# Kernel tuning notes

Hardware: AMD Instinct MI355X
Metric: run time of the kernel (lower is better)

## Reference

```python
import jax, jax.numpy as jnp
import numpy as np

DIM = 512      # dim_token
H = 8          # nheads
EH = DIM // H  # head dim
MAXT = 512     # max_time_id
NBUCK = 2 * MAXT - 1  # relative-position buckets


def rope(x, t):
    # x: [N,H,L,E], t: [N,L] integer time ids
    half = x.shape[-1] // 2
    inv_freq = 1.0 / (10000.0 ** (jnp.arange(half, dtype=jnp.float32) / half))
    ang = t.astype(jnp.float32)[:, None, :, None] * inv_freq  # [N,1,L,half]
    cos, sin = jnp.cos(ang), jnp.sin(ang)
    x1, x2 = x[..., :half], x[..., half:]
    return jnp.concatenate([x1 * cos - x2 * sin, x2 * cos + x1 * sin], axis=-1)


def setup_inputs() -> dict:
    key = jax.random.key(0)
    ks = jax.random.split(key, 8)
    N, L = 4, 1024
    x = jax.random.normal(ks[0], (N, L, DIM), dtype=jnp.float32)
    mask = jnp.ones((N, L), dtype=bool)
    time_ids = jnp.sort(jax.random.randint(ks[1], (N, L), 0, MAXT), axis=-1)
    s = DIM ** -0.5
    W_in = jax.random.normal(ks[2], (3 * DIM, DIM), dtype=jnp.float32) * s
    b_in = jnp.zeros((3 * DIM,), dtype=jnp.float32)
    W_out = jax.random.normal(ks[3], (DIM, DIM), dtype=jnp.float32) * s
    b_out = jnp.zeros((DIM,), dtype=jnp.float32)
    rel_table = jax.random.normal(ks[4], (H, NBUCK), dtype=jnp.float32) * 0.02
    post_table = jax.random.normal(ks[5], (H, NBUCK), dtype=jnp.float32) * 0.02
    return dict(x=x, mask=mask, time_ids=time_ids, W_in=W_in, b_in=b_in,
                W_out=W_out, b_out=b_out, rel_table=rel_table, post_table=post_table)


def reference(x, mask, time_ids, W_in, b_in, W_out, b_out, rel_table, post_table):
    N, L, _ = x.shape
    # 1. input projection, chunk into q,k,v
    qkv = x @ W_in.T + b_in
    q, k, v = jnp.split(qkv, 3, axis=-1)
    split = lambda t: t.reshape(N, L, H, EH).transpose(0, 2, 1, 3)  # [N,H,L,EH]
    q, k, v = split(q), split(k), split(v)
    # 2. RoPE on q,k using time_ids (pe_module.apply_attention_pe)
    q = rope(q, time_ids)
    k = rope(k, time_ids)
    # relative time-difference bucket indices [N,L,L]
    diff = time_ids[:, :, None] - time_ids[:, None, :]
    idx = jnp.clip(diff + (MAXT - 1), 0, NBUCK - 1)
    bias = rel_table[:, idx].transpose(1, 0, 2, 3)        # [N,H,L,L] pre-softmax bias
    post_bias = post_table[:, idx].transpose(1, 0, 2, 3)  # [N,H,L,L] EfficientRPE post-softmax
    # 3. manual attention path (bias is not None -> bypass SDPA)
    scale = EH ** -0.5
    scores = jnp.einsum('bhqe,bhke->bhqk', q, k) * scale + bias
    am = mask[:, None, None, :]  # [N,1,1,L]
    scores = jnp.where(am, scores, -jnp.inf)
    w = jax.nn.softmax(scores, axis=-1)
    out = jnp.einsum('bhqk,bhke->bhqe', w, v)
    # EfficientRPE post-softmax correction
    post_bias = jnp.where(am, post_bias, 0.0)
    out = out + jnp.einsum('bhql,bhle->bhqe', post_bias, v)
    # 4. merge heads + output projection
    out = out.transpose(0, 2, 1, 3).reshape(N, L, DIM)
    return out @ W_out.T + b_out
```

## Files before the change

### kernel.cpp

```cpp
#include <hip/hip_runtime.h>
#include <hip/hip_bf16.h>

#define BB 4
#define LL 1024
#define DIMD 512
#define HH 8
#define EHD 64
#define NBUCK 1023

using f32x4 = __attribute__((ext_vector_type(4))) float;
using s16x8 = __attribute__((ext_vector_type(8))) short;

__device__ __forceinline__ ushort to_bf16(float x) {
    union { float f; unsigned u; } v; v.f = x;
    unsigned r = (v.u + 0x7FFFu + ((v.u >> 16) & 1u)) >> 16;
    return (ushort)r;
}

__device__ __forceinline__ unsigned cvt_pk_bf16(float lo, float hi) {
    unsigned r;
    asm("v_cvt_pk_bf16_f32 %0, %1, %2" : "=v"(r) : "v"(lo), "v"(hi));
    return r;
}

__device__ __forceinline__ void gl_lds16(const ushort* g, ushort* l) {
    __builtin_amdgcn_global_load_lds(
        (const __attribute__((address_space(1))) unsigned int*)g,
        (__attribute__((address_space(3))) unsigned int*)l, 16, 0, 0);
}

#define XN  2097152
#define WIN 786432
#define WON 262144
__global__ __launch_bounds__(256) void prep_all(const float* __restrict__ x,
                                                const float* __restrict__ wi,
                                                const float* __restrict__ wo,
                                                ushort* __restrict__ xb,
                                                ushort* __restrict__ wib,
                                                ushort* __restrict__ wob,
                                                float2* __restrict__ rtab)
{
    if (blockIdx.x < 3072) {
        int idx = (blockIdx.x * 256 + threadIdx.x) * 4;
        const float* src; ushort* dst; int off;
        if (idx < XN)            { src = x;  dst = xb;  off = idx; }
        else if (idx < XN + WIN) { src = wi; dst = wib; off = idx - XN; }
        else                     { src = wo; dst = wob; off = idx - XN - WIN; }
        float4 v = *(const float4*)&src[off];
        ushort4 o;
        o.x = to_bf16(v.x); o.y = to_bf16(v.y);
        o.z = to_bf16(v.z); o.w = to_bf16(v.w);
        *(ushort4*)&dst[off] = o;
    } else {
        int idx = (blockIdx.x - 3072) * 256 + threadIdx.x;
        int tt = idx >> 5, e = idx & 31;
        const float L2T = 13.287712379549449f;
        float inv = exp2f(-(float)e * (L2T / 32.f));
        float ang = (float)tt * inv;
        float s, c;
        sincosf(ang, &s, &c);
        rtab[idx] = make_float2(c, s);
    }
}

template<int BN, int WMODE>
__global__ __launch_bounds__(256) void mfma_gemm(const ushort* __restrict__ A,
                                                 const ushort* __restrict__ B,
                                                 const float* __restrict__ bias,
                                                 float* __restrict__ outf,
                                                 ushort* __restrict__ outq,
                                                 ushort* __restrict__ outk,
                                                 ushort* __restrict__ outv,
                                                 const int* __restrict__ time_ids,
                                                 const float2* __restrict__ rtab,
                                                 int M, int N, int K)
{
    constexpr int NREP = BN / 32;
    constexpr int BUFU = 8192 + BN * 64;
    __shared__ __align__(16) char smem[2 * BUFU * 2];
    ushort* base = (ushort*)smem;

    const int t = threadIdx.x;
    const int lane = t & 63;
    const int w = t >> 6;
    const int l15 = lane & 15, lg = lane >> 4;
    const int wr = w >> 1, wc = w & 1;
    const int m0 = blockIdx.x * 128;
    const int n0 = blockIdx.y * BN;

    const int asub = lane >> 3;
    const int kc8 = (lane & 7) * 8;
    const int arow_base = w * 32;
    const int brow_base = w * (BN / 4);

    f32x4 acc[4][NREP];
    #pragma unroll
    for (int mf = 0; mf < 4; ++mf)
        #pragma unroll
        for (int nf = 0; nf < NREP; ++nf)
            acc[mf][nf] = {0.f, 0.f, 0.f, 0.f};

    #define STAGE_G(BUF, K0)                                                          \
        do {                                                                          \
            ushort* Ab = base + (BUF) * BUFU;                                         \
            ushort* Bb = Ab + 8192;                                                   \
            _Pragma("unroll")                                                         \
            for (int i = 0; i < 4; ++i) {                                             \
                int row = arow_base + i * 8;                                          \
                gl_lds16(&A[(size_t)(m0 + row + asub) * K + (K0) + kc8], &Ab[row * 64]); \
            }                                                                         \
            _Pragma("unroll")                                                         \
            for (int i = 0; i < BN / 32; ++i) {                                       \
                int row = brow_base + i * 8;                                          \
                gl_lds16(&B[(size_t)(n0 + row + asub) * K + (K0) + kc8], &Bb[row * 64]); \
            }                                                                         \
        } while (0)

    STAGE_G(0, 0);
    __syncthreads();

    for (int k0 = 0; k0 < K; k0 += 64) {
        const int buf = (k0 >> 6) & 1;
        if (k0 + 64 < K) {
            STAGE_G(buf ^ 1, k0 + 64);
            if constexpr (BN == 128) asm volatile("s_waitcnt vmcnt(8)" ::: "memory");
            else                     asm volatile("s_waitcnt vmcnt(6)" ::: "memory");
        } else {
            asm volatile("s_waitcnt vmcnt(0)" ::: "memory");
        }
        __builtin_amdgcn_s_barrier();
        ushort* Abuf = base + buf * BUFU;
        ushort* Bbuf = Abuf + 8192;
        #pragma unroll
        for (int kk = 0; kk < 2; ++kk) {
            s16x8 af[4], bf[NREP];
            #pragma unroll
            for (int mf = 0; mf < 4; ++mf)
                af[mf] = *(const s16x8*)&Abuf[(wr * 64 + mf * 16 + l15) * 64 + kk * 32 + lg * 8];
            #pragma unroll
            for (int nf = 0; nf < NREP; ++nf)
                bf[nf] = *(const s16x8*)&Bbuf[(wc * (BN / 2) + nf * 16 + l15) * 64 + kk * 32 + lg * 8];
            __builtin_amdgcn_s_setprio(1);
            #pragma unroll
            for (int mf = 0; mf < 4; ++mf)
                #pragma unroll
                for (int nf = 0; nf < NREP; ++nf)
                    acc[mf][nf] = __builtin_amdgcn_mfma_f32_16x16x32_bf16(af[mf], bf[nf], acc[mf][nf], 0, 0, 0);
            __builtin_amdgcn_s_setprio(0);
        }
        asm volatile("" ::: "memory");
        __builtin_amdgcn_s_barrier();
    }

    if (WMODE == 0) {
        float bv[NREP];
        #pragma unroll
        for (int nf = 0; nf < NREP; ++nf) bv[nf] = bias[n0 + wc * (BN / 2) + nf * 16 + l15];
        #pragma unroll
        for (int mf = 0; mf < 4; ++mf)
            #pragma unroll
            for (int r = 0; r < 4; ++r) {
                int m = m0 + wr * 64 + mf * 16 + lg * 4 + r;
                #pragma unroll
                for (int nf = 0; nf < NREP; ++nf)
                    outf[(size_t)m * N + n0 + wc * (BN / 2) + nf * 16 + l15] = acc[mf][nf][r] + bv[nf];
            }
    } else {
        const int which = n0 >> 9;
        if (which < 2) {
            const int h = ((n0 & 511) + wc * 64) >> 6;
            ushort* dst = (which == 0) ? outq : outk;
            float bv[4];
            #pragma unroll
            for (int nf = 0; nf < 4; ++nf) bv[nf] = bias[n0 + wc * 64 + nf * 16 + l15];
            #pragma unroll
            for (int mf = 0; mf < 4; ++mf)
                #pragma unroll
                for (int r = 0; r < 4; ++r) {
                    int m = m0 + wr * 64 + mf * 16 + lg * 4 + r;
                    int b = m >> 10, li = m & (LL - 1);
                    int tt = time_ids[b * LL + li];
                    size_t rowbase = (((size_t)(b * HH + h)) * LL + li) * EHD;
                    #pragma unroll
                    for (int nf = 0; nf < 2; ++nf) {
                        float2 cs = rtab[tt * 32 + nf * 16 + l15];
                        float v1 = acc[mf][nf][r] + bv[nf];
                        float v2 = acc[mf][nf + 2][r] + bv[nf + 2];
                        dst[rowbase + nf * 16 + l15]      = to_bf16(v1 * cs.x - v2 * cs.y);
                        dst[rowbase + 32 + nf * 16 + l15] = to_bf16(v2 * cs.x + v1 * cs.y);
                    }
                }
        } else {
            ushort* T = (ushort*)smem;
            float bv[4];
            #pragma unroll
            for (int nf = 0; nf < 4; ++nf) bv[nf] = bias[n0 + wc * 64 + nf * 16 + l15];
            #pragma unroll
            for (int mf = 0; mf < 4; ++mf)
                #pragma unroll
                for (int nf = 0; nf < 4; ++nf) {
                    int n = wc * 64 + nf * 16 + l15;
                    int mb = wr * 64 + mf * 16 + lg * 4;
                    ushort4 pk;
                    pk.x = to_bf16(acc[mf][nf][0] + bv[nf]);
                    pk.y = to_bf16(acc[mf][nf][1] + bv[nf]);
                    pk.z = to_bf16(acc[mf][nf][2] + bv[nf]);
                    pk.w = to_bf16(acc[mf][nf][3] + bv[nf]);
                    *(ushort4*)&T[n * 136 + mb] = pk;
                }
            __syncthreads();
            const int b = m0 >> 10, li0 = m0 & (LL - 1);
            const int hbase = (n0 & 511) >> 6;
            #pragma unroll
            for (int it = 0; it < 8; ++it) {
                int n = it * 16 + (t >> 4);
                int mc = (t & 15) * 8;
                uint4 val = *(const uint4*)&T[n * 136 + mc];
                int h = hbase + (n >> 6);
                int e = n & 63;
                *(uint4*)&outv[(((size_t)(b * HH + h)) * EHD + e) * LL + li0 + mc] = val;
            }
        }
    }
}

__global__ __launch_bounds__(512, 4) void attn_mfma(const ushort* __restrict__ qb,
                                                    const ushort* __restrict__ kb,
                                                    const ushort* __restrict__ vt,
                                                    const int* __restrict__ time_ids,
                                                    const float* __restrict__ rel_table,
                                                    const float* __restrict__ post_table,
                                                    ushort* __restrict__ ao)
{
    __shared__ __align__(16) char smem[65536];
    __shared__ __align__(16) float rt_s[1024];
    __shared__ __align__(16) float pt_s[1024];
    __shared__ __align__(16) int   tid4_s[1024];

    const int t = threadIdx.x;
    const int lane = t & 63;
    const int w = t >> 6;
    const int wh = w & 3;
    const int half = w >> 2;
    const int l15 = lane & 15, lg = lane >> 4;

    const int wg = blockIdx.x;
    const int xcd = wg & 7;
    const int j = wg >> 3;
    const int bh = xcd * 4 + (j & 3);
    const int qt = j >> 2;
    const int b = bh >> 3, h = bh & 7;
    const int wq0 = qt * 64 + wh * 16;

    ushort* Kh = (ushort*)smem + half * 8192;
    ushort* Vh = (ushort*)(smem + 32768) + half * 8192;

    const float L2E = 1.4426950408889634f;
    const float M0 = 12.0f;
    for (int i = t; i < NBUCK; i += 512) {
        rt_s[i] = rel_table[h * NBUCK + i] * L2E - M0;
        pt_s[i] = post_table[h * NBUCK + i];
    }
    const int* tid_b = time_ids + b * LL;
    #pragma unroll
    for (int i = 0; i < 2; ++i) tid4_s[i * 512 + t] = tid_b[i * 512 + t] * 4;

    const ushort* qpan = qb + (size_t)bh * LL * EHD;
    const ushort* kpan = kb + (size_t)bh * LL * EHD;
    const ushort* vpan = vt + (size_t)bh * EHD * LL;

    s16x8 qf[2];
    #pragma unroll
    for (int ec = 0; ec < 2; ++ec)
        qf[ec] = *(const s16x8*)&qpan[(size_t)(wq0 + l15) * EHD + ec * 32 + lg * 8];

    const int tqA4 = (tid_b[wq0 + l15] + 511) * 4;

    const int srow = lane >> 3;
    const int sswz = (lane & 7) ^ srow;

    #define STAGE(BUF, K0)                                                        \
        do {                                                                      \
            int r0 = wh * 8 + srow;                                               \
            gl_lds16(&kpan[(size_t)((K0) + r0) * EHD + sswz * 8],      &Kh[(BUF) * 4096 + wh * 8 * 64]);        \
            gl_lds16(&vpan[(size_t)r0 * LL + (K0) + sswz * 8],         &Vh[(BUF) * 4096 + wh * 8 * 64]);        \
            gl_lds16(&kpan[(size_t)((K0) + r0 + 32) * EHD + sswz * 8], &Kh[(BUF) * 4096 + (32 + wh * 8) * 64]); \
            gl_lds16(&vpan[(size_t)(r0 + 32) * LL + (K0) + sswz * 8],  &Vh[(BUF) * 4096 + (32 + wh * 8) * 64]); \
        } while (0)

    float dreg = 0.f;
    f32x4 ot[4], o2[4];
    #pragma unroll
    for (int ei = 0; ei < 4; ++ei) {
        ot[ei] = {0.f, 0.f, 0.f, 0.f};
        o2[ei] = {0.f, 0.f, 0.f, 0.f};
    }

    const int ktbase = half * 8;
    STAGE(0, ktbase * 64);
    __syncthreads();

    const int srcA = ((lg & 1) << 5) + l15;
    const bool hi = (lg & 2) != 0;

    for (int i = 0; i < 8; ++i) {
        const int cur = i & 1;
        const int k0 = (ktbase + i) * 64;
        if (i < 7) {
            STAGE(cur ^ 1, k0 + 64);
            asm volatile("s_waitcnt vmcnt(4)" ::: "memory");
        } else {
            asm volatile("s_waitcnt vmcnt(0)" ::: "memory");
        }
        __builtin_amdgcn_s_barrier();

        const char* Kc = (const char*)&Kh[cur * 4096];
        const char* Vc = (const char*)&Vh[cur * 4096];

        f32x4 sc[4];
        #pragma unroll
        for (int ci = 0; ci < 4; ++ci) sc[ci] = {0.f, 0.f, 0.f, 0.f};
        __builtin_amdgcn_s_setprio(1);
        #pragma unroll
        for (int ec = 0; ec < 2; ++ec)
            #pragma unroll
            for (int ci = 0; ci < 4; ++ci) {
                int row = ci * 16 + l15;
                s16x8 kf = *(const s16x8*)(Kc + row * 128 +
                                           ((ec * 64 + lg * 16) ^ ((row & 7) << 4)));
                sc[ci] = __builtin_amdgcn_mfma_f32_16x16x32_bf16(kf, qf[ec], sc[ci], 0, 0, 0);
            }
        __builtin_amdgcn_s_setprio(0);

        s16x8 vf[4][2];
        #pragma unroll
        for (int ei = 0; ei < 4; ++ei)
            #pragma unroll
            for (int kk = 0; kk < 2; ++kk) {
                int row = ei * 16 + l15;
                vf[ei][kk] = *(const s16x8*)(Vc + row * 128 +
                                             ((kk * 64 + lg * 16) ^ ((row & 7) << 4)));
            }

        #pragma unroll
        for (int kk = 0; kk < 2; ++kk) {
            int4 ta = *(const int4*)&tid4_s[k0 + kk * 32 + lg * 8];
            int4 tb = *(const int4*)&tid4_s[k0 + kk * 32 + lg * 8 + 4];
            float p0 = *(const float*)((const char*)pt_s + (tqA4 - ta.x));
            float p1 = *(const float*)((const char*)pt_s + (tqA4 - ta.y));
            float p2 = *(const float*)((const char*)pt_s + (tqA4 - ta.z));
            float p3 = *(const float*)((const char*)pt_s + (tqA4 - ta.w));
            float p4 = *(const float*)((const char*)pt_s + (tqA4 - tb.x));
            float p5 = *(const float*)((const char*)pt_s + (tqA4 - tb.y));
            float p6 = *(const float*)((const char*)pt_s + (tqA4 - tb.z));
            float p7 = *(const float*)((const char*)pt_s + (tqA4 - tb.w));
            union { unsigned u[4]; s16x8 v; } pbu;
            pbu.u[0] = cvt_pk_bf16(p0, p1);
            pbu.u[1] = cvt_pk_bf16(p2, p3);
            pbu.u[2] = cvt_pk_bf16(p4, p5);
            pbu.u[3] = cvt_pk_bf16(p6, p7);
            __builtin_amdgcn_s_setprio(1);
            #pragma unroll
            for (int ei = 0; ei < 4; ++ei)
                o2[ei] = __builtin_amdgcn_mfma_f32_16x16x32_bf16(vf[ei][kk], pbu.v, o2[ei], 0, 0, 0);
            __builtin_amdgcn_s_setprio(0);
        }

        float rsum = 0.f;
        #pragma unroll
        for (int ci = 0; ci < 4; ++ci) {
            int4 tk4 = *(const int4*)&tid4_s[k0 + ci * 16 + lg * 4];
            float p0 = exp2f(sc[ci][0] * 0.18033688011111793f + *(const float*)((const char*)rt_s + (tqA4 - tk4.x)));
            float p1 = exp2f(sc[ci][1] * 0.18033688011111793f + *(const float*)((const char*)rt_s + (tqA4 - tk4.y)));
            float p2 = exp2f(sc[ci][2] * 0.18033688011111793f + *(const float*)((const char*)rt_s + (tqA4 - tk4.z)));
            float p3 = exp2f(sc[ci][3] * 0.18033688011111793f + *(const float*)((const char*)rt_s + (tqA4 - tk4.w)));
            sc[ci][0] = p0; sc[ci][1] = p1; sc[ci][2] = p2; sc[ci][3] = p3;
            rsum += (p0 + p1) + (p2 + p3);
        }
        dreg += rsum;

        unsigned pk[4][2];
        #pragma unroll
        for (int ci = 0; ci < 4; ++ci) {
            pk[ci][0] = cvt_pk_bf16(sc[ci][0], sc[ci][1]);
            pk[ci][1] = cvt_pk_bf16(sc[ci][2], sc[ci][3]);
        }

        #pragma unroll
        for (int kk = 0; kk < 2; ++kk) {
            unsigned a0 = __shfl(pk[kk * 2][0], srcA),      b0 = __shfl(pk[kk * 2 + 1][0], srcA);
            unsigned a1 = __shfl(pk[kk * 2][1], srcA),      b1 = __shfl(pk[kk * 2 + 1][1], srcA);
            unsigned a2 = __shfl(pk[kk * 2][0], srcA + 16), b2 = __shfl(pk[kk * 2 + 1][0], srcA + 16);
            unsigned a3 = __shfl(pk[kk * 2][1], srcA + 16), b3 = __shfl(pk[kk * 2 + 1][1], srcA + 16);
            union { unsigned u[4]; s16x8 v; } pb;
            pb.u[0] = hi ? b0 : a0;
            pb.u[1] = hi ? b1 : a1;
            pb.u[2] = hi ? b2 : a2;
            pb.u[3] = hi ? b3 : a3;
            __builtin_amdgcn_s_setprio(1);
            #pragma unroll
            for (int ei = 0; ei < 4; ++ei)
                ot[ei] = __builtin_amdgcn_mfma_f32_16x16x32_bf16(vf[ei][kk], pb.v, ot[ei], 0, 0, 0);
            __builtin_amdgcn_s_setprio(0);
        }

        asm volatile("" ::: "memory");
        __builtin_amdgcn_s_barrier();
    }

    dreg += __shfl_xor(dreg, 16);
    dreg += __shfl_xor(dreg, 32);

    float* mergeO = (float*)smem;
    float* mergeB = (float*)(smem + 17408);
    float* mergeD = (float*)(smem + 34816);
    const int mrow = wh * 16 + l15;

    if (half == 1) {
        #pragma unroll
        for (int ei = 0; ei < 4; ++ei) {
            *(float4*)&mergeO[mrow * 68 + ei * 16 + lg * 4] =
                make_float4(ot[ei][0], ot[ei][1], ot[ei][2], ot[ei][3]);
            *(float4*)&mergeB[mrow * 68 + ei * 16 + lg * 4] =
                make_float4(o2[ei][0], o2[ei][1], o2[ei][2], o2[ei][3]);
        }
        if (lg == 0) mergeD[mrow] = dreg;
    }
    __syncthreads();

    if (half == 0) {
        float invd = 1.f / (dreg + mergeD[mrow]);
        const size_t orow = (size_t)(b * LL + wq0 + l15) * DIMD + h * EHD;
        #pragma unroll
        for (int ei = 0; ei < 4; ++ei) {
            float4 o1 = *(const float4*)&mergeO[mrow * 68 + ei * 16 + lg * 4];
            float4 b1 = *(const float4*)&mergeB[mrow * 68 + ei * 16 + lg * 4];
            ushort4 st;
            st.x = to_bf16((ot[ei][0] + o1.x) * invd + o2[ei][0] + b1.x);
            st.y = to_bf16((ot[ei][1] + o1.y) * invd + o2[ei][1] + b1.y);
            st.z = to_bf16((ot[ei][2] + o1.z) * invd + o2[ei][2] + b1.z);
            st.w = to_bf16((ot[ei][3] + o1.w) * invd + o2[ei][3] + b1.w);
            *(ushort4*)&ao[orow + ei * 16 + lg * 4] = st;
        }
    }
}

extern "C" void kernel_launch(void* const* d_in, const int* in_sizes, int n_in,
                              void* d_out, int out_size, void* d_ws, size_t ws_size,
                              hipStream_t stream)
{
    const float* x        = (const float*)d_in[0];
    const int*   time_ids = (const int*)d_in[2];
    const float* W_in     = (const float*)d_in[3];
    const float* b_in     = (const float*)d_in[4];
    const float* W_out    = (const float*)d_in[5];
    const float* b_out    = (const float*)d_in[6];
    const float* rel_t    = (const float*)d_in[7];
    const float* post_t   = (const float*)d_in[8];
    float* out = (float*)d_out;

    ushort* wsu = (ushort*)d_ws;
    ushort* xb  = wsu;
    ushort* wib = xb + XN;
    ushort* wob = wib + WIN;
    ushort* qbf = wob + WON;
    ushort* kbf = qbf + XN;
    ushort* vtb = kbf + XN;
    ushort* aob = vtb + XN;
    float2* rtab = (float2*)(aob + XN);

    prep_all<<<3136, 256, 0, stream>>>(x, W_in, W_out, xb, wib, wob, rtab);
    mfma_gemm<128, 1><<<dim3(32, 12), 256, 0, stream>>>(xb, wib, b_in,
                                                        nullptr, qbf, kbf, vtb,
                                                        time_ids, (const float2*)rtab,
                                                        BB * LL, 3 * DIMD, DIMD);
    attn_mfma<<<512, 512, 0, stream>>>(qbf, kbf, vtb, time_ids,
                                       rel_t, post_t, aob);
    mfma_gemm<64, 0><<<dim3(32, 8), 256, 0, stream>>>(aob, wob, b_out,
                                                      out, nullptr, nullptr, nullptr,
                                                      nullptr, nullptr,
                                                      BB * LL, DIMD, DIMD);
}
```

Baseline: 64.64 us.

## Process two 16-row query groups per wave to reuse K/V LDS fragments

Each wave now handles 32 query rows (two groups of 16) instead of 16, so every K and V fragment read from LDS feeds twice as many MFMAs. The grid is halved to 256 blocks and the launch bound drops to 2 blocks per CU to make room for the doubled accumulators and K fragments held in registers. The intent is to cut LDS traffic and K/V staging per unit of work, at the cost of higher register pressure, fewer blocks than CUs, and a serialized two-pass merge epilogue.

```diff
diff --git a/kernel.cpp b/kernel.cpp
--- a/kernel.cpp
+++ b/kernel.cpp
@@ -224,7 +224,7 @@
     }
 }
 
-__global__ __launch_bounds__(512, 4) void attn_mfma(const ushort* __restrict__ qb,
+__global__ __launch_bounds__(512, 2) void attn_mfma(const ushort* __restrict__ qb,
                                                     const ushort* __restrict__ kb,
                                                     const ushort* __restrict__ vt,
                                                     const int* __restrict__ time_ids,
@@ -250,7 +250,7 @@
     const int bh = xcd * 4 + (j & 3);
     const int qt = j >> 2;
     const int b = bh >> 3, h = bh & 7;
-    const int wq0 = qt * 64 + wh * 16;
+    const int wq0 = qt * 128 + wh * 32;
 
     ushort* Kh = (ushort*)smem + half * 8192;
     ushort* Vh = (ushort*)(smem + 32768) + half * 8192;
@@ -269,12 +269,15 @@
     const ushort* kpan = kb + (size_t)bh * LL * EHD;
     const ushort* vpan = vt + (size_t)bh * EHD * LL;
 
-    s16x8 qf[2];
+    s16x8 qf[2][2];
     #pragma unroll
-    for (int ec = 0; ec < 2; ++ec)
-        qf[ec] = *(const s16x8*)&qpan[(size_t)(wq0 + l15) * EHD + ec * 32 + lg * 8];
-
-    const int tqA4 = (tid_b[wq0 + l15] + 511) * 4;
+    for (int g = 0; g < 2; ++g)
+        #pragma unroll
+        for (int ec = 0; ec < 2; ++ec)
+            qf[g][ec] = *(const s16x8*)&qpan[(size_t)(wq0 + g * 16 + l15) * EHD + ec * 32 + lg * 8];
+
+    const int tqA4[2] = {(tid_b[wq0 + l15] + 511) * 4,
+                         (tid_b[wq0 + 16 + l15] + 511) * 4};
 
     const int srow = lane >> 3;
     const int sswz = (lane & 7) ^ srow;
@@ -288,13 +291,15 @@
             gl_lds16(&vpan[(size_t)(r0 + 32) * LL + (K0) + sswz * 8],  &Vh[(BUF) * 4096 + (32 + wh * 8) * 64]); \
         } while (0)
 
-    float dreg = 0.f;
-    f32x4 ot[4], o2[4];
+    float dreg[2] = {0.f, 0.f};
+    f32x4 ot[2][4], o2[2][4];
     #pragma unroll
-    for (int ei = 0; ei < 4; ++ei) {
-        ot[ei] = {0.f, 0.f, 0.f, 0.f};
-        o2[ei] = {0.f, 0.f, 0.f, 0.f};
-    }
+    for (int g = 0; g < 2; ++g)
+        #pragma unroll
+        for (int ei = 0; ei < 4; ++ei) {
+            ot[g][ei] = {0.f, 0.f, 0.f, 0.f};
+            o2[g][ei] = {0.f, 0.f, 0.f, 0.f};
+        }
 
     const int ktbase = half * 8;
     STAGE(0, ktbase * 64);
@@ -317,19 +322,29 @@
         const char* Kc = (const char*)&Kh[cur * 4096];
         const char* Vc = (const char*)&Vh[cur * 4096];
 
-        f32x4 sc[4];
-        #pragma unroll
-        for (int ci = 0; ci < 4; ++ci) sc[ci] = {0.f, 0.f, 0.f, 0.f};
+        s16x8 kf[4][2];
+        #pragma unroll
+        for (int ci = 0; ci < 4; ++ci)
+            #pragma unroll
+            for (int ec = 0; ec < 2; ++ec) {
+                int row = ci * 16 + l15;
+                kf[ci][ec] = *(const s16x8*)(Kc + row * 128 +
+                                             ((ec * 64 + lg * 16) ^ ((row & 7) << 4)));
+            }
+
+        f32x4 sc[2][4];
+        #pragma unroll
+        for (int g = 0; g < 2; ++g)
+            #pragma unroll
+            for (int ci = 0; ci < 4; ++ci) sc[g][ci] = {0.f, 0.f, 0.f, 0.f};
         __builtin_amdgcn_s_setprio(1);
         #pragma unroll
         for (int ec = 0; ec < 2; ++ec)
             #pragma unroll
-            for (int ci = 0; ci < 4; ++ci) {
-                int row = ci * 16 + l15;
-                s16x8 kf = *(const s16x8*)(Kc + row * 128 +
-                                           ((ec * 64 + lg * 16) ^ ((row & 7) << 4)));
-                sc[ci] = __builtin_amdgcn_mfma_f32_16x16x32_bf16(kf, qf[ec], sc[ci], 0, 0, 0);
-            }
+            for (int ci = 0; ci < 4; ++ci)
+                #pragma unroll
+                for (int g = 0; g < 2; ++g)
+                    sc[g][ci] = __builtin_amdgcn_mfma_f32_16x16x32_bf16(kf[ci][ec], qf[g][ec], sc[g][ci], 0, 0, 0);
         __builtin_amdgcn_s_setprio(0);
 
         s16x8 vf[4][2];
@@ -346,101 +361,118 @@
         for (int kk = 0; kk < 2; ++kk) {
             int4 ta = *(const int4*)&tid4_s[k0 + kk * 32 + lg * 8];
             int4 tb = *(const int4*)&tid4_s[k0 + kk * 32 + lg * 8 + 4];
-            float p0 = *(const float*)((const char*)pt_s + (tqA4 - ta.x));
-            float p1 = *(const float*)((const char*)pt_s + (tqA4 - ta.y));
-            float p2 = *(const float*)((const char*)pt_s + (tqA4 - ta.z));
-            float p3 = *(const float*)((const char*)pt_s + (tqA4 - ta.w));
-            float p4 = *(const float*)((const char*)pt_s + (tqA4 - tb.x));
-            float p5 = *(const float*)((const char*)pt_s + (tqA4 - tb.y));
-            float p6 = *(const float*)((const char*)pt_s + (tqA4 - tb.z));
-            float p7 = *(const float*)((const char*)pt_s + (tqA4 - tb.w));
-            union { unsigned u[4]; s16x8 v; } pbu;
-            pbu.u[0] = cvt_pk_bf16(p0, p1);
-            pbu.u[1] = cvt_pk_bf16(p2, p3);
-            pbu.u[2] = cvt_pk_bf16(p4, p5);
-            pbu.u[3] = cvt_pk_bf16(p6, p7);
-            __builtin_amdgcn_s_setprio(1);
-            #pragma unroll
-            for (int ei = 0; ei < 4; ++ei)
-                o2[ei] = __builtin_amdgcn_mfma_f32_16x16x32_bf16(vf[ei][kk], pbu.v, o2[ei], 0, 0, 0);
-            __builtin_amdgcn_s_setprio(0);
-        }
-
-        float rsum = 0.f;
+            #pragma unroll
+            for (int g = 0; g < 2; ++g) {
+                float p0 = *(const float*)((const char*)pt_s + (tqA4[g] - ta.x));
+                float p1 = *(const float*)((const char*)pt_s + (tqA4[g] - ta.y));
+                float p2 = *(const float*)((const char*)pt_s + (tqA4[g] - ta.z));
+                float p3 = *(const float*)((const char*)pt_s + (tqA4[g] - ta.w));
+                float p4 = *(const float*)((const char*)pt_s + (tqA4[g] - tb.x));
+                float p5 = *(const float*)((const char*)pt_s + (tqA4[g] - tb.y));
+                float p6 = *(const float*)((const char*)pt_s + (tqA4[g] - tb.z));
+                float p7 = *(const float*)((const char*)pt_s + (tqA4[g] - tb.w));
+                union { unsigned u[4]; s16x8 v; } pbu;
+                pbu.u[0] = cvt_pk_bf16(p0, p1);
+                pbu.u[1] = cvt_pk_bf16(p2, p3);
+                pbu.u[2] = cvt_pk_bf16(p4, p5);
+                pbu.u[3] = cvt_pk_bf16(p6, p7);
+                __builtin_amdgcn_s_setprio(1);
+                #pragma unroll
+                for (int ei = 0; ei < 4; ++ei)
+                    o2[g][ei] = __builtin_amdgcn_mfma_f32_16x16x32_bf16(vf[ei][kk], pbu.v, o2[g][ei], 0, 0, 0);
+                __builtin_amdgcn_s_setprio(0);
+            }
+        }
+
+        float rsum[2] = {0.f, 0.f};
         #pragma unroll
         for (int ci = 0; ci < 4; ++ci) {
             int4 tk4 = *(const int4*)&tid4_s[k0 + ci * 16 + lg * 4];
-            float p0 = exp2f(sc[ci][0] * 0.18033688011111793f + *(const float*)((const char*)rt_s + (tqA4 - tk4.x)));
-            float p1 = exp2f(sc[ci][1] * 0.18033688011111793f + *(const float*)((const char*)rt_s + (tqA4 - tk4.y)));
-            float p2 = exp2f(sc[ci][2] * 0.18033688011111793f + *(const float*)((const char*)rt_s + (tqA4 - tk4.z)));
-            float p3 = exp2f(sc[ci][3] * 0.18033688011111793f + *(const float*)((const char*)rt_s + (tqA4 - tk4.w)));
-            sc[ci][0] = p0; sc[ci][1] = p1; sc[ci][2] = p2; sc[ci][3] = p3;
-            rsum += (p0 + p1) + (p2 + p3);
-        }
-        dreg += rsum;
-
-        unsigned pk[4][2];
-        #pragma unroll
-        for (int ci = 0; ci < 4; ++ci) {
-            pk[ci][0] = cvt_pk_bf16(sc[ci][0], sc[ci][1]);
-            pk[ci][1] = cvt_pk_bf16(sc[ci][2], sc[ci][3]);
-        }
-
-        #pragma unroll
-        for (int kk = 0; kk < 2; ++kk) {
-            unsigned a0 = __shfl(pk[kk * 2][0], srcA),      b0 = __shfl(pk[kk * 2 + 1][0], srcA);
-            unsigned a1 = __shfl(pk[kk * 2][1], srcA),      b1 = __shfl(pk[kk * 2 + 1][1], srcA);
-            unsigned a2 = __shfl(pk[kk * 2][0], srcA + 16), b2 = __shfl(pk[kk * 2 + 1][0], srcA + 16);
-            unsigned a3 = __shfl(pk[kk * 2][1], srcA + 16), b3 = __shfl(pk[kk * 2 + 1][1], srcA + 16);
-            union { unsigned u[4]; s16x8 v; } pb;
-            pb.u[0] = hi ? b0 : a0;
-            pb.u[1] = hi ? b1 : a1;
-            pb.u[2] = hi ? b2 : a2;
-            pb.u[3] = hi ? b3 : a3;
-            __builtin_amdgcn_s_setprio(1);
-            #pragma unroll
-            for (int ei = 0; ei < 4; ++ei)
-                ot[ei] = __builtin_amdgcn_mfma_f32_16x16x32_bf16(vf[ei][kk], pb.v, ot[ei], 0, 0, 0);
-            __builtin_amdgcn_s_setprio(0);
-        }
+            #pragma unroll
+            for (int g = 0; g < 2; ++g) {
+                float p0 = exp2f(sc[g][ci][0] * 0.18033688011111793f + *(const float*)((const char*)rt_s + (tqA4[g] - tk4.x)));
+                float p1 = exp2f(sc[g][ci][1] * 0.18033688011111793f + *(const float*)((const char*)rt_s + (tqA4[g] - tk4.y)));
+                float p2 = exp2f(sc[g][ci][2] * 0.18033688011111793f + *(const float*)((const char*)rt_s + (tqA4[g] - tk4.z)));
+                float p3 = exp2f(sc[g][ci][3] * 0.18033688011111793f + *(const float*)((const char*)rt_s + (tqA4[g] - tk4.w)));
+                sc[g][ci][0] = p0; sc[g][ci][1] = p1; sc[g][ci][2] = p2; sc[g][ci][3] = p3;
+                rsum[g] += (p0 + p1) + (p2 + p3);
+            }
+        }
+        dreg[0] += rsum[0];
+        dreg[1] += rsum[1];
+
+        unsigned pk[2][4][2];
+        #pragma unroll
+        for (int g = 0; g < 2; ++g)
+            #pragma unroll
+            for (int ci = 0; ci < 4; ++ci) {
+                pk[g][ci][0] = cvt_pk_bf16(sc[g][ci][0], sc[g][ci][1]);
+                pk[g][ci][1] = cvt_pk_bf16(sc[g][ci][2], sc[g][ci][3]);
+            }
+
+        #pragma unroll
+        for (int g = 0; g < 2; ++g)
+            #pragma unroll
+            for (int kk = 0; kk < 2; ++kk) {
+                unsigned a0 = __shfl(pk[g][kk * 2][0], srcA),      b0 = __shfl(pk[g][kk * 2 + 1][0], srcA);
+                unsigned a1 = __shfl(pk[g][kk * 2][1], srcA),      b1 = __shfl(pk[g][kk * 2 + 1][1], srcA);
+                unsigned a2 = __shfl(pk[g][kk * 2][0], srcA + 16), b2 = __shfl(pk[g][kk * 2 + 1][0], srcA + 16);
+                unsigned a3 = __shfl(pk[g][kk * 2][1], srcA + 16), b3 = __shfl(pk[g][kk * 2 + 1][1], srcA + 16);
+                union { unsigned u[4]; s16x8 v; } pb;
+                pb.u[0] = hi ? b0 : a0;
+                pb.u[1] = hi ? b1 : a1;
+                pb.u[2] = hi ? b2 : a2;
+                pb.u[3] = hi ? b3 : a3;
+                __builtin_amdgcn_s_setprio(1);
+                #pragma unroll
+                for (int ei = 0; ei < 4; ++ei)
+                    ot[g][ei] = __builtin_amdgcn_mfma_f32_16x16x32_bf16(vf[ei][kk], pb.v, ot[g][ei], 0, 0, 0);
+                __builtin_amdgcn_s_setprio(0);
+            }
 
         asm volatile("" ::: "memory");
         __builtin_amdgcn_s_barrier();
     }
 
-    dreg += __shfl_xor(dreg, 16);
-    dreg += __shfl_xor(dreg, 32);
+    #pragma unroll
+    for (int g = 0; g < 2; ++g) {
+        dreg[g] += __shfl_xor(dreg[g], 16);
+        dreg[g] += __shfl_xor(dreg[g], 32);
+    }
 
     float* mergeO = (float*)smem;
     float* mergeB = (float*)(smem + 17408);
     float* mergeD = (float*)(smem + 34816);
     const int mrow = wh * 16 + l15;
 
-    if (half == 1) {
-        #pragma unroll
-        for (int ei = 0; ei < 4; ++ei) {
-            *(float4*)&mergeO[mrow * 68 + ei * 16 + lg * 4] =
-                make_float4(ot[ei][0], ot[ei][1], ot[ei][2], ot[ei][3]);
-            *(float4*)&mergeB[mrow * 68 + ei * 16 + lg * 4] =
-                make_float4(o2[ei][0], o2[ei][1], o2[ei][2], o2[ei][3]);
-        }
-        if (lg == 0) mergeD[mrow] = dreg;
-    }
-    __syncthreads();
-
-    if (half == 0) {
-        float invd = 1.f / (dreg + mergeD[mrow]);
-        const size_t orow = (size_t)(b * LL + wq0 + l15) * DIMD + h * EHD;
-        #pragma unroll
-        for (int ei = 0; ei < 4; ++ei) {
-            float4 o1 = *(const float4*)&mergeO[mrow * 68 + ei * 16 + lg * 4];
-            float4 b1 = *(const float4*)&mergeB[mrow * 68 + ei * 16 + lg * 4];
-            ushort4 st;
-            st.x = to_bf16((ot[ei][0] + o1.x) * invd + o2[ei][0] + b1.x);
-            st.y = to_bf16((ot[ei][1] + o1.y) * invd + o2[ei][1] + b1.y);
-            st.z = to_bf16((ot[ei][2] + o1.z) * invd + o2[ei][2] + b1.z);
-            st.w = to_bf16((ot[ei][3] + o1.w) * invd + o2[ei][3] + b1.w);
-            *(ushort4*)&ao[orow + ei * 16 + lg * 4] = st;
+    #pragma unroll
+    for (int g = 0; g < 2; ++g) {
+        __syncthreads();
+        if (half == 1) {
+            #pragma unroll
+            for (int ei = 0; ei < 4; ++ei) {
+                *(float4*)&mergeO[mrow * 68 + ei * 16 + lg * 4] =
+                    make_float4(ot[g][ei][0], ot[g][ei][1], ot[g][ei][2], ot[g][ei][3]);
+                *(float4*)&mergeB[mrow * 68 + ei * 16 + lg * 4] =
+                    make_float4(o2[g][ei][0], o2[g][ei][1], o2[g][ei][2], o2[g][ei][3]);
+            }
+            if (lg == 0) mergeD[mrow] = dreg[g];
+        }
+        __syncthreads();
+        if (half == 0) {
+            float invd = 1.f / (dreg[g] + mergeD[mrow]);
+            const size_t orow = (size_t)(b * LL + wq0 + g * 16 + l15) * DIMD + h * EHD;
+            #pragma unroll
+            for (int ei = 0; ei < 4; ++ei) {
+                float4 o1 = *(const float4*)&mergeO[mrow * 68 + ei * 16 + lg * 4];
+                float4 b1 = *(const float4*)&mergeB[mrow * 68 + ei * 16 + lg * 4];
+                ushort4 st;
+                st.x = to_bf16((ot[g][ei][0] + o1.x) * invd + o2[g][ei][0] + b1.x);
+                st.y = to_bf16((ot[g][ei][1] + o1.y) * invd + o2[g][ei][1] + b1.y);
+                st.z = to_bf16((ot[g][ei][2] + o1.z) * invd + o2[g][ei][2] + b1.z);
+                st.w = to_bf16((ot[g][ei][3] + o1.w) * invd + o2[g][ei][3] + b1.w);
+                *(ushort4*)&ao[orow + ei * 16 + lg * 4] = st;
+            }
         }
     }
 }
@@ -474,7 +506,7 @@
                                                         nullptr, qbf, kbf, vtb,
                                                         time_ids, (const float2*)rtab,
                                                         BB * LL, 3 * DIMD, DIMD);
-    attn_mfma<<<512, 512, 0, stream>>>(qbf, kbf, vtb, time_ids,
+    attn_mfma<<<256, 512, 0, stream>>>(qbf, kbf, vtb, time_ids,
                                        rel_t, post_t, aob);
     mfma_gemm<64, 0><<<dim3(32, 8), 256, 0, stream>>>(aob, wob, b_out,
                                                       out, nullptr, nullptr, nullptr,
```

Measured after the change: 64.11 us, median of 2. About the same (-0.8%).

## Drop split-K across wave halves in attention; 4 waves each cover full key range

Applied to the files above, without the earlier changes.

The attention kernel previously used 8 waves per block, with two halves each processing half of the keys and merging partial outputs through shared memory. Now each block has 4 waves that walk all 1024 keys, staging 128-key double-buffered tiles and processing two 64-key sub-tiles per barrier. This removes the cross-half LDS merge and halves the number of barriers per key. In exchange each wave does twice the serial work and the block has fewer waves to hide latency.

```diff
diff --git a/kernel.cpp b/kernel.cpp
--- a/kernel.cpp
+++ b/kernel.cpp
@@ -224,7 +224,7 @@
     }
 }
 
-__global__ __launch_bounds__(512, 4) void attn_mfma(const ushort* __restrict__ qb,
+__global__ __launch_bounds__(256, 2) void attn_mfma(const ushort* __restrict__ qb,
                                                     const ushort* __restrict__ kb,
                                                     const ushort* __restrict__ vt,
                                                     const int* __restrict__ time_ids,
@@ -232,7 +232,8 @@
                                                     const float* __restrict__ post_table,
                                                     ushort* __restrict__ ao)
 {
-    __shared__ __align__(16) char smem[65536];
+    __shared__ __align__(16) ushort Kbuf[2][8192];
+    __shared__ __align__(16) ushort Vbuf[2][8192];
     __shared__ __align__(16) float rt_s[1024];
     __shared__ __align__(16) float pt_s[1024];
     __shared__ __align__(16) int   tid4_s[1024];
@@ -240,8 +241,6 @@
     const int t = threadIdx.x;
     const int lane = t & 63;
     const int w = t >> 6;
-    const int wh = w & 3;
-    const int half = w >> 2;
     const int l15 = lane & 15, lg = lane >> 4;
 
     const int wg = blockIdx.x;
@@ -250,20 +249,17 @@
     const int bh = xcd * 4 + (j & 3);
     const int qt = j >> 2;
     const int b = bh >> 3, h = bh & 7;
-    const int wq0 = qt * 64 + wh * 16;
-
-    ushort* Kh = (ushort*)smem + half * 8192;
-    ushort* Vh = (ushort*)(smem + 32768) + half * 8192;
+    const int wq0 = qt * 64 + w * 16;
 
     const float L2E = 1.4426950408889634f;
     const float M0 = 12.0f;
-    for (int i = t; i < NBUCK; i += 512) {
+    for (int i = t; i < NBUCK; i += 256) {
         rt_s[i] = rel_table[h * NBUCK + i] * L2E - M0;
         pt_s[i] = post_table[h * NBUCK + i];
     }
     const int* tid_b = time_ids + b * LL;
     #pragma unroll
-    for (int i = 0; i < 2; ++i) tid4_s[i * 512 + t] = tid_b[i * 512 + t] * 4;
+    for (int i = 0; i < 4; ++i) tid4_s[i * 256 + t] = tid_b[i * 256 + t] * 4;
 
     const ushort* qpan = qb + (size_t)bh * LL * EHD;
     const ushort* kpan = kb + (size_t)bh * LL * EHD;
@@ -279,13 +275,22 @@
     const int srow = lane >> 3;
     const int sswz = (lane & 7) ^ srow;
 
-    #define STAGE(BUF, K0)                                                        \
-        do {                                                                      \
-            int r0 = wh * 8 + srow;                                               \
-            gl_lds16(&kpan[(size_t)((K0) + r0) * EHD + sswz * 8],      &Kh[(BUF) * 4096 + wh * 8 * 64]);        \
-            gl_lds16(&vpan[(size_t)r0 * LL + (K0) + sswz * 8],         &Vh[(BUF) * 4096 + wh * 8 * 64]);        \
-            gl_lds16(&kpan[(size_t)((K0) + r0 + 32) * EHD + sswz * 8], &Kh[(BUF) * 4096 + (32 + wh * 8) * 64]); \
-            gl_lds16(&vpan[(size_t)(r0 + 32) * LL + (K0) + sswz * 8],  &Vh[(BUF) * 4096 + (32 + wh * 8) * 64]); \
+    #define STAGE(BUF, K0)                                                              \
+        do {                                                                            \
+            _Pragma("unroll")                                                           \
+            for (int rr = 0; rr < 4; ++rr) {                                            \
+                int r0 = w * 8 + srow + rr * 32;                                        \
+                gl_lds16(&kpan[(size_t)((K0) + r0) * EHD + sswz * 8],                   \
+                         &Kbuf[BUF][(w * 8 + rr * 32) * 64]);                           \
+            }                                                                           \
+            _Pragma("unroll")                                                           \
+            for (int ks = 0; ks < 2; ++ks)                                              \
+                _Pragma("unroll")                                                       \
+                for (int eg = 0; eg < 2; ++eg) {                                        \
+                    int e0 = w * 8 + srow + eg * 32;                                    \
+                    gl_lds16(&vpan[(size_t)e0 * LL + (K0) + ks * 64 + sswz * 8],        \
+                             &Vbuf[BUF][ks * 4096 + (w * 8 + eg * 32) * 64]);           \
+                }                                                                       \
         } while (0)
 
     float dreg = 0.f;
@@ -296,112 +301,115 @@
         o2[ei] = {0.f, 0.f, 0.f, 0.f};
     }
 
-    const int ktbase = half * 8;
-    STAGE(0, ktbase * 64);
+    STAGE(0, 0);
     __syncthreads();
 
     const int srcA = ((lg & 1) << 5) + l15;
     const bool hi = (lg & 2) != 0;
 
-    for (int i = 0; i < 8; ++i) {
-        const int cur = i & 1;
-        const int k0 = (ktbase + i) * 64;
-        if (i < 7) {
-            STAGE(cur ^ 1, k0 + 64);
-            asm volatile("s_waitcnt vmcnt(4)" ::: "memory");
+    for (int it = 0; it < 8; ++it) {
+        const int buf = it & 1;
+        const int kbase = it * 128;
+        if (it < 7) {
+            STAGE(buf ^ 1, kbase + 128);
+            asm volatile("s_waitcnt vmcnt(8)" ::: "memory");
         } else {
             asm volatile("s_waitcnt vmcnt(0)" ::: "memory");
         }
         __builtin_amdgcn_s_barrier();
 
-        const char* Kc = (const char*)&Kh[cur * 4096];
-        const char* Vc = (const char*)&Vh[cur * 4096];
-
-        f32x4 sc[4];
         #pragma unroll
-        for (int ci = 0; ci < 4; ++ci) sc[ci] = {0.f, 0.f, 0.f, 0.f};
-        __builtin_amdgcn_s_setprio(1);
-        #pragma unroll
-        for (int ec = 0; ec < 2; ++ec)
+        for (int ks = 0; ks < 2; ++ks) {
+            const int k0 = kbase + ks * 64;
+            const char* Kc = (const char*)&Kbuf[buf][ks * 4096];
+            const char* Vc = (const char*)&Vbuf[buf][ks * 4096];
+
+            f32x4 sc[4];
+            #pragma unroll
+            for (int ci = 0; ci < 4; ++ci) sc[ci] = {0.f, 0.f, 0.f, 0.f};
+            __builtin_amdgcn_s_setprio(1);
+            #pragma unroll
+            for (int ec = 0; ec < 2; ++ec)
+                #pragma unroll
+                for (int ci = 0; ci < 4; ++ci) {
+                    int row = ci * 16 + l15;
+                    s16x8 kf = *(const s16x8*)(Kc + row * 128 +
+                                               ((ec * 64 + lg * 16) ^ ((row & 7) << 4)));
+                    sc[ci] = __builtin_amdgcn_mfma_f32_16x16x32_bf16(kf, qf[ec], sc[ci], 0, 0, 0);
+                }
+            __builtin_amdgcn_s_setprio(0);
+
+            s16x8 vf[4][2];
+            #pragma unroll
+            for (int ei = 0; ei < 4; ++ei)
+                #pragma unroll
+                for (int kk = 0; kk < 2; ++kk) {
+                    int row = ei * 16 + l15;
+                    vf[ei][kk] = *(const s16x8*)(Vc + row * 128 +
+                                                 ((kk * 64 + lg * 16) ^ ((row & 7) << 4)));
+                }
+
+            #pragma unroll
+            for (int kk = 0; kk < 2; ++kk) {
+                int4 ta = *(const int4*)&tid4_s[k0 + kk * 32 + lg * 8];
+                int4 tb = *(const int4*)&tid4_s[k0 + kk * 32 + lg * 8 + 4];
+                float p0 = *(const float*)((const char*)pt_s + (tqA4 - ta.x));
+                float p1 = *(const float*)((const char*)pt_s + (tqA4 - ta.y));
+                float p2 = *(const float*)((const char*)pt_s + (tqA4 - ta.z));
+                float p3 = *(const float*)((const char*)pt_s + (tqA4 - ta.w));
+                float p4 = *(const float*)((const char*)pt_s + (tqA4 - tb.x));
+                float p5 = *(const float*)((const char*)pt_s + (tqA4 - tb.y));
+                float p6 = *(const float*)((const char*)pt_s + (tqA4 - tb.z));
+                float p7 = *(const float*)((const char*)pt_s + (tqA4 - tb.w));
+                union { unsigned u[4]; s16x8 v; } pbu;
+                pbu.u[0] = cvt_pk_bf16(p0, p1);
+                pbu.u[1] = cvt_pk_bf16(p2, p3);
+                pbu.u[2] = cvt_pk_bf16(p4, p5);
+                pbu.u[3] = cvt_pk_bf16(p6, p7);
+                __builtin_amdgcn_s_setprio(1);
+                #pragma unroll
+                for (int ei = 0; ei < 4; ++ei)
+                    o2[ei] = __builtin_amdgcn_mfma_f32_16x16x32_bf16(vf[ei][kk], pbu.v, o2[ei], 0, 0, 0);
+                __builtin_amdgcn_s_setprio(0);
+            }
+
+            float rsum = 0.f;
             #pragma unroll
             for (int ci = 0; ci < 4; ++ci) {
-                int row = ci * 16 + l15;
-                s16x8 kf = *(const s16x8*)(Kc + row * 128 +
-                                           ((ec * 64 + lg * 16) ^ ((row & 7) << 4)));
-                sc[ci] = __builtin_amdgcn_mfma_f32_16x16x32_bf16(kf, qf[ec], sc[ci], 0, 0, 0);
-            }
-        __builtin_amdgcn_s_setprio(0);
-
-        s16x8 vf[4][2];
-        #pragma unroll
-        for (int ei = 0; ei < 4; ++ei)
+                int4 tk4 = *(const int4*)&tid4_s[k0 + ci * 16 + lg * 4];
+                float p0 = exp2f(sc[ci][0] * 0.18033688011111793f + *(const float*)((const char*)rt_s + (tqA4 - tk4.x)));
+                float p1 = exp2f(sc[ci][1] * 0.18033688011111793f + *(const float*)((const char*)rt_s + (tqA4 - tk4.y)));
+                float p2 = exp2f(sc[ci][2] * 0.18033688011111793f + *(const float*)((const char*)rt_s + (tqA4 - tk4.z)));
+                float p3 = exp2f(sc[ci][3] * 0.18033688011111793f + *(const float*)((const char*)rt_s + (tqA4 - tk4.w)));
+                sc[ci][0] = p0; sc[ci][1] = p1; sc[ci][2] = p2; sc[ci][3] = p3;
+                rsum += (p0 + p1) + (p2 + p3);
+            }
+            dreg += rsum;
+
+            unsigned pk[4][2];
+            #pragma unroll
+            for (int ci = 0; ci < 4; ++ci) {
+                pk[ci][0] = cvt_pk_bf16(sc[ci][0], sc[ci][1]);
+                pk[ci][1] = cvt_pk_bf16(sc[ci][2], sc[ci][3]);
+            }
+
             #pragma unroll
             for (int kk = 0; kk < 2; ++kk) {
-                int row = ei * 16 + l15;
-                vf[ei][kk] = *(const s16x8*)(Vc + row * 128 +
-                                             ((kk * 64 + lg * 16) ^ ((row & 7) << 4)));
-            }
-
-        #pragma unroll
-        for (int kk = 0; kk < 2; ++kk) {
-            int4 ta = *(const int4*)&tid4_s[k0 + kk * 32 + lg * 8];
-            int4 tb = *(const int4*)&tid4_s[k0 + kk * 32 + lg * 8 + 4];
-            float p0 = *(const float*)((const char*)pt_s + (tqA4 - ta.x));
-            float p1 = *(const float*)((const char*)pt_s + (tqA4 - ta.y));
-            float p2 = *(const float*)((const char*)pt_s + (tqA4 - ta.z));
-            float p3 = *(const float*)((const char*)pt_s + (tqA4 - ta.w));
-            float p4 = *(const float*)((const char*)pt_s + (tqA4 - tb.x));
-            float p5 = *(const float*)((const char*)pt_s + (tqA4 - tb.y));
-            float p6 = *(const float*)((const char*)pt_s + (tqA4 - tb.z));
-            float p7 = *(const float*)((const char*)pt_s + (tqA4 - tb.w));
-            union { unsigned u[4]; s16x8 v; } pbu;
-            pbu.u[0] = cvt_pk_bf16(p0, p1);
-            pbu.u[1] = cvt_pk_bf16(p2, p3);
-            pbu.u[2] = cvt_pk_bf16(p4, p5);
-            pbu.u[3] = cvt_pk_bf16(p6, p7);
-            __builtin_amdgcn_s_setprio(1);
-            #pragma unroll
-            for (int ei = 0; ei < 4; ++ei)
-                o2[ei] = __builtin_amdgcn_mfma_f32_16x16x32_bf16(vf[ei][kk], pbu.v, o2[ei], 0, 0, 0);
-            __builtin_amdgcn_s_setprio(0);
-        }
-
-        float rsum = 0.f;
-        #pragma unroll
-        for (int ci = 0; ci < 4; ++ci) {
-            int4 tk4 = *(const int4*)&tid4_s[k0 + ci * 16 + lg * 4];
-            float p0 = exp2f(sc[ci][0] * 0.18033688011111793f + *(const float*)((const char*)rt_s + (tqA4 - tk4.x)));
-            float p1 = exp2f(sc[ci][1] * 0.18033688011111793f + *(const float*)((const char*)rt_s + (tqA4 - tk4.y)));
-            float p2 = exp2f(sc[ci][2] * 0.18033688011111793f + *(const float*)((const char*)rt_s + (tqA4 - tk4.z)));
-            float p3 = exp2f(sc[ci][3] * 0.18033688011111793f + *(const float*)((const char*)rt_s + (tqA4 - tk4.w)));
-            sc[ci][0] = p0; sc[ci][1] = p1; sc[ci][2] = p2; sc[ci][3] = p3;
-            rsum += (p0 + p1) + (p2 + p3);
-        }
-        dreg += rsum;
-
-        unsigned pk[4][2];
-        #pragma unroll
-        for (int ci = 0; ci < 4; ++ci) {
-            pk[ci][0] = cvt_pk_bf16(sc[ci][0], sc[ci][1]);
-            pk[ci][1] = cvt_pk_bf16(sc[ci][2], sc[ci][3]);
-        }
-
-        #pragma unroll
-        for (int kk = 0; kk < 2; ++kk) {
-            unsigned a0 = __shfl(pk[kk * 2][0], srcA),      b0 = __shfl(pk[kk * 2 + 1][0], srcA);
-            unsigned a1 = __shfl(pk[kk * 2][1], srcA),      b1 = __shfl(pk[kk * 2 + 1][1], srcA);
-            unsigned a2 = __shfl(pk[kk * 2][0], srcA + 16), b2 = __shfl(pk[kk * 2 + 1][0], srcA + 16);
-            unsigned a3 = __shfl(pk[kk * 2][1], srcA + 16), b3 = __shfl(pk[kk * 2 + 1][1], srcA + 16);
-            union { unsigned u[4]; s16x8 v; } pb;
-            pb.u[0] = hi ? b0 : a0;
-            pb.u[1] = hi ? b1 : a1;
-            pb.u[2] = hi ? b2 : a2;
-            pb.u[3] = hi ? b3 : a3;
-            __builtin_amdgcn_s_setprio(1);
-            #pragma unroll
-            for (int ei = 0; ei < 4; ++ei)
-                ot[ei] = __builtin_amdgcn_mfma_f32_16x16x32_bf16(vf[ei][kk], pb.v, ot[ei], 0, 0, 0);
-            __builtin_amdgcn_s_setprio(0);
+                unsigned a0 = __shfl(pk[kk * 2][0], srcA),      b0 = __shfl(pk[kk * 2 + 1][0], srcA);
+                unsigned a1 = __shfl(pk[kk * 2][1], srcA),      b1 = __shfl(pk[kk * 2 + 1][1], srcA);
+                unsigned a2 = __shfl(pk[kk * 2][0], srcA + 16), b2 = __shfl(pk[kk * 2 + 1][0], srcA + 16);
+                unsigned a3 = __shfl(pk[kk * 2][1], srcA + 16), b3 = __shfl(pk[kk * 2 + 1][1], srcA + 16);
+                union { unsigned u[4]; s16x8 v; } pb;
+                pb.u[0] = hi ? b0 : a0;
+                pb.u[1] = hi ? b1 : a1;
+                pb.u[2] = hi ? b2 : a2;
+                pb.u[3] = hi ? b3 : a3;
+                __builtin_amdgcn_s_setprio(1);
+                #pragma unroll
+                for (int ei = 0; ei < 4; ++ei)
+                    ot[ei] = __builtin_amdgcn_mfma_f32_16x16x32_bf16(vf[ei][kk], pb.v, ot[ei], 0, 0, 0);
+                __builtin_amdgcn_s_setprio(0);
+            }
         }
 
         asm volatile("" ::: "memory");
@@ -411,37 +419,16 @@
     dreg += __shfl_xor(dreg, 16);
     dreg += __shfl_xor(dreg, 32);
 
-    float* mergeO = (float*)smem;
-    float* mergeB = (float*)(smem + 17408);
-    float* mergeD = (float*)(smem + 34816);
-    const int mrow = wh * 16 + l15;
-
-    if (half == 1) {
-        #pragma unroll
-        for (int ei = 0; ei < 4; ++ei) {
-            *(float4*)&mergeO[mrow * 68 + ei * 16 + lg * 4] =
-                make_float4(ot[ei][0], ot[ei][1], ot[ei][2], ot[ei][3]);
-            *(float4*)&mergeB[mrow * 68 + ei * 16 + lg * 4] =
-                make_float4(o2[ei][0], o2[ei][1], o2[ei][2], o2[ei][3]);
-        }
-        if (lg == 0) mergeD[mrow] = dreg;
-    }
-    __syncthreads();
-
-    if (half == 0) {
-        float invd = 1.f / (dreg + mergeD[mrow]);
-        const size_t orow = (size_t)(b * LL + wq0 + l15) * DIMD + h * EHD;
-        #pragma unroll
-        for (int ei = 0; ei < 4; ++ei) {
-            float4 o1 = *(const float4*)&mergeO[mrow * 68 + ei * 16 + lg * 4];
-            float4 b1 = *(const float4*)&mergeB[mrow * 68 + ei * 16 + lg * 4];
-            ushort4 st;
-            st.x = to_bf16((ot[ei][0] + o1.x) * invd + o2[ei][0] + b1.x);
-            st.y = to_bf16((ot[ei][1] + o1.y) * invd + o2[ei][1] + b1.y);
-            st.z = to_bf16((ot[ei][2] + o1.z) * invd + o2[ei][2] + b1.z);
-            st.w = to_bf16((ot[ei][3] + o1.w) * invd + o2[ei][3] + b1.w);
-            *(ushort4*)&ao[orow + ei * 16 + lg * 4] = st;
-        }
+    const float invd = 1.f / dreg;
+    const size_t orow = (size_t)(b * LL + wq0 + l15) * DIMD + h * EHD;
+    #pragma unroll
+    for (int ei = 0; ei < 4; ++ei) {
+        ushort4 st;
+        st.x = to_bf16(ot[ei][0] * invd + o2[ei][0]);
+        st.y = to_bf16(ot[ei][1] * invd + o2[ei][1]);
+        st.z = to_bf16(ot[ei][2] * invd + o2[ei][2]);
+        st.w = to_bf16(ot[ei][3] * invd + o2[ei][3]);
+        *(ushort4*)&ao[orow + ei * 16 + lg * 4] = st;
     }
 }
 
@@ -474,7 +461,7 @@
                                                         nullptr, qbf, kbf, vtb,
                                                         time_ids, (const float2*)rtab,
                                                         BB * LL, 3 * DIMD, DIMD);
-    attn_mfma<<<512, 512, 0, stream>>>(qbf, kbf, vtb, time_ids,
+    attn_mfma<<<512, 256, 0, stream>>>(qbf, kbf, vtb, time_ids,
                                        rel_t, post_t, aob);
     mfma_gemm<64, 0><<<dim3(32, 8), 256, 0, stream>>>(aob, wob, b_out,
                                                       out, nullptr, nullptr, nullptr,
```

Measured after the change: 65.33 us. About the same (+1.1%).
